# Kernel tuning notes

Hardware: AMD Instinct MI355X
Metric: run time of the kernel (lower is better)

## Reference

```python
import jax, jax.numpy as jnp
import numpy as np

EMBED_DIM = 768
N_HEADS = 12
HEAD_DIM = EMBED_DIM // N_HEADS
B, T = 2, 4096


def setup_inputs() -> dict:
    key = jax.random.key(0)
    k1, k2, k3, k4, k5 = jax.random.split(key, 5)
    s = 1.0 / np.sqrt(EMBED_DIM)
    return {
        "x": jax.random.normal(k1, (B, T, EMBED_DIM), dtype=jnp.float32),
        "Wqkv": jax.random.normal(k2, (EMBED_DIM, 3 * EMBED_DIM), dtype=jnp.float32) * s,
        "bqkv": jnp.zeros((3 * EMBED_DIM,), dtype=jnp.float32),
        "Wproj": jax.random.normal(k3, (EMBED_DIM, EMBED_DIM), dtype=jnp.float32) * s,
        "bproj": jnp.zeros((EMBED_DIM,), dtype=jnp.float32),
    }


def reference(x, Wqkv, bqkv, Wproj, bproj):
    Bz, Tz, C = x.shape
    qkv = x @ Wqkv + bqkv                         # [B,T,3C]
    q, k, v = jnp.split(qkv, 3, axis=2)
    # [B,T,H,D] -> [B,H,T,D]
    def heads(t):
        return t.reshape(Bz, Tz, N_HEADS, HEAD_DIM).transpose(0, 2, 1, 3)
    q, k, v = heads(q), heads(k), heads(v)
    scale = 1.0 / np.sqrt(HEAD_DIM)
    att = jnp.einsum("bhqd,bhkd->bhqk", q, k) * scale   # [B,H,T,T]
    causal = jnp.tril(jnp.ones((Tz, Tz), dtype=bool))
    att = jnp.where(causal[None, None], att, -jnp.inf)
    att = jax.nn.softmax(att, axis=-1)
    y = jnp.einsum("bhqk,bhkd->bhqd", att, v)            # [B,H,T,D]
    y = y.transpose(0, 2, 1, 3).reshape(Bz, Tz, C)
    return y @ Wproj + bproj
```

## Files before the change

kernel.cpp:

```cpp
#include <hip/hip_runtime.h>
#include <math.h>
#include <stdint.h>

typedef __attribute__((ext_vector_type(8))) short bf16x8;
typedef __attribute__((ext_vector_type(4))) float f32x4;

__device__ __forceinline__ unsigned short f2bf(float f) {
    union { float f; unsigned u; } v; v.f = f;
    return (unsigned short)((v.u + 0x7fffu + ((v.u >> 16) & 1u)) >> 16);
}

__device__ __forceinline__ unsigned pkbf(float a, float b) {
    union { float f; unsigned u; } x, y; x.f = a; y.f = b;
    return ((y.u + 0x8000u) & 0xffff0000u) | ((x.u + 0x8000u) >> 16);
}

__global__ void k_convert(const float* __restrict__ in, unsigned short* __restrict__ out, int n4) {
    int i = blockIdx.x * blockDim.x + threadIdx.x;
    if (i >= n4) return;
    float4 f = ((const float4*)in)[i];
    ushort4 o;
    o.x = f2bf(f.x); o.y = f2bf(f.y); o.z = f2bf(f.z); o.w = f2bf(f.w);
    ((ushort4*)out)[i] = o;
}

__global__ void k_transpose(const float* __restrict__ in, unsigned short* __restrict__ out, int R, int C) {
    __shared__ float tile[32][33];
    int c0 = blockIdx.x * 32, r0 = blockIdx.y * 32;
    int tx = threadIdx.x, ty = threadIdx.y;
#pragma unroll
    for (int i = 0; i < 4; ++i)
        tile[ty + i * 8][tx] = in[(size_t)(r0 + ty + i * 8) * C + c0 + tx];
    __syncthreads();
#pragma unroll
    for (int i = 0; i < 4; ++i)
        out[(size_t)(c0 + ty + i * 8) * R + r0 + tx] = f2bf(tile[tx][ty + i * 8]);
}

#define LDT 40

__device__ __forceinline__ void gemm_core(
    const unsigned short* __restrict__ A, const unsigned short* __restrict__ Bt,
    int K, unsigned short* As, unsigned short* Bs, f32x4 (&acc)[4][4])
{
    const int tid  = threadIdx.x;
    const int lane = tid & 63;
    const int w    = tid >> 6;
    const int wm   = (w >> 1) * 64, wn = (w & 1) * 64;
    const int l15  = lane & 15, quad = lane >> 4;
    const int m0 = blockIdx.x * 128, n0 = blockIdx.y * 128;

    const f32x4 zero = {0.f, 0.f, 0.f, 0.f};
#pragma unroll
    for (int i = 0; i < 4; ++i)
#pragma unroll
        for (int j = 0; j < 4; ++j) acc[i][j] = zero;

    const int r0 = tid >> 2, p8 = (tid & 3) * 8;
    const unsigned short* Ag0 = A  + (size_t)(m0 + r0) * K + p8;
    const unsigned short* Ag1 = A  + (size_t)(m0 + r0 + 64) * K + p8;
    const unsigned short* Bg0 = Bt + (size_t)(n0 + r0) * K + p8;
    const unsigned short* Bg1 = Bt + (size_t)(n0 + r0 + 64) * K + p8;

    int4 a0 = *(const int4*)Ag0;
    int4 a1 = *(const int4*)Ag1;
    int4 b0 = *(const int4*)Bg0;
    int4 b1 = *(const int4*)Bg1;

    const int nk = K >> 5;
    for (int kt = 0; kt < nk; ++kt) {
        __syncthreads();
        *(int4*)&As[r0 * LDT + p8]        = a0;
        *(int4*)&As[(r0 + 64) * LDT + p8] = a1;
        *(int4*)&Bs[r0 * LDT + p8]        = b0;
        *(int4*)&Bs[(r0 + 64) * LDT + p8] = b1;
        __syncthreads();
        if (kt + 1 < nk) {
            int koff = (kt + 1) * 32;
            a0 = *(const int4*)(Ag0 + koff);
            a1 = *(const int4*)(Ag1 + koff);
            b0 = *(const int4*)(Bg0 + koff);
            b1 = *(const int4*)(Bg1 + koff);
        }
        bf16x8 af[4], bfr[4];
#pragma unroll
        for (int mi = 0; mi < 4; ++mi)
            af[mi] = *(const bf16x8*)&As[(wm + mi * 16 + l15) * LDT + quad * 8];
#pragma unroll
        for (int nj = 0; nj < 4; ++nj)
            bfr[nj] = *(const bf16x8*)&Bs[(wn + nj * 16 + l15) * LDT + quad * 8];
#pragma unroll
        for (int mi = 0; mi < 4; ++mi)
#pragma unroll
            for (int nj = 0; nj < 4; ++nj)
                acc[mi][nj] = __builtin_amdgcn_mfma_f32_16x16x32_bf16(af[mi], bfr[nj], acc[mi][nj], 0, 0, 0);
    }
}

__global__ __launch_bounds__(256) void k_gemm_qkv(
    const unsigned short* __restrict__ A, const unsigned short* __restrict__ Bt,
    const float* __restrict__ bias,
    unsigned short* __restrict__ QL, unsigned short* __restrict__ KL,
    unsigned short* __restrict__ VL)
{
    __shared__ __align__(16) unsigned short As[128 * LDT];
    __shared__ __align__(16) unsigned short Bs[128 * LDT];
    f32x4 acc[4][4];
    gemm_core(A, Bt, 768, As, Bs, acc);

    const int tid = threadIdx.x, lane = tid & 63, w = tid >> 6;
    const int wm = (w >> 1) * 64, wn = (w & 1) * 64;
    const int l15 = lane & 15, quad = lane >> 4;
    const int m0 = blockIdx.x * 128, n0 = blockIdx.y * 128;
    const float cscale = 0.18033688011f;
#pragma unroll
    for (int nj = 0; nj < 4; ++nj) {
        int cg = n0 + wn + nj * 16 + l15;
        float bv = bias[cg];
        int which = cg / 768;
        int rem = cg - which * 768;
        int hd = rem >> 6, d = rem & 63;
        float sc = (which == 0) ? cscale : 1.0f;
#pragma unroll
        for (int mi = 0; mi < 4; ++mi) {
#pragma unroll
            for (int r = 0; r < 4; ++r) {
                int rg = m0 + wm + mi * 16 + quad * 4 + r;
                int b = rg >> 12, tk = rg & 4095;
                int bh = b * 12 + hd;
                unsigned short ob = f2bf((acc[mi][nj][r] + bv) * sc);
                if (which == 0) {
                    size_t idx = ((((size_t)bh * 128 + (tk >> 5)) * 2 + ((tk >> 4) & 1)) * 2 + (d >> 5)) * 512
                               + ((d >> 3) & 3) * 128 + (tk & 15) * 8 + (d & 7);
                    QL[idx] = ob;
                } else if (which == 1) {
                    size_t idx = ((((size_t)bh * 64 + (tk >> 6)) * 4 + ((tk >> 4) & 3)) * 2 + (d >> 5)) * 512
                               + ((d >> 3) & 3) * 128 + (tk & 15) * 8 + (d & 7);
                    KL[idx] = ob;
                } else {
                    int wi = tk & 63;
                    size_t idx = ((((size_t)bh * 64 + (tk >> 6)) * 4 + (d >> 4)) * 2 + (wi >> 5)) * 512
                               + ((wi >> 3) & 3) * 128 + (d & 15) * 8 + (wi & 7);
                    VL[idx] = ob;
                }
            }
        }
    }
}

__global__ __launch_bounds__(256) void k_gemm_proj(
    const unsigned short* __restrict__ A, const unsigned short* __restrict__ Bt,
    const float* __restrict__ bias, float* __restrict__ out)
{
    __shared__ __align__(16) unsigned short As[128 * LDT];
    __shared__ __align__(16) unsigned short Bs[128 * LDT];
    f32x4 acc[4][4];
    gemm_core(A, Bt, 768, As, Bs, acc);

    const int tid = threadIdx.x, lane = tid & 63, w = tid >> 6;
    const int wm = (w >> 1) * 64, wn = (w & 1) * 64;
    const int l15 = lane & 15, quad = lane >> 4;
    const int m0 = blockIdx.x * 128, n0 = blockIdx.y * 128;
#pragma unroll
    for (int nj = 0; nj < 4; ++nj) {
        int cg = n0 + wn + nj * 16 + l15;
        float bv = bias[cg];
#pragma unroll
        for (int mi = 0; mi < 4; ++mi)
#pragma unroll
            for (int r = 0; r < 4; ++r) {
                int rg = m0 + wm + mi * 16 + quad * 4 + r;
                out[(size_t)rg * 768 + cg] = acc[mi][nj][r] + bv;
            }
    }
}

#define LDP 68

__global__ __launch_bounds__(256) void k_attn(
    const unsigned short* __restrict__ QL, const unsigned short* __restrict__ KL,
    const unsigned short* __restrict__ VL, unsigned short* __restrict__ Y)
{
    __shared__ __align__(16) char smem[30720];
    unsigned short* Ps = (unsigned short*)smem;
    float* Cb = (float*)smem;

    const int tid = threadIdx.x, lane = tid & 63, w = tid >> 6;
    const int l15 = lane & 15, quad = lane >> 4;
    const int id = blockIdx.x;
    const int bh = id % 24;
    const int qi = 127 - id / 24;
    const int q0 = qi * 32;
    const int nkt = qi / 2 + 1;
    const int lo = (nkt * w) >> 2, hi = (nkt * (w + 1)) >> 2;
    unsigned short* Pw = Ps + w * 32 * LDP;

    const unsigned short* Qb = QL + (((size_t)bh * 128 + qi) * 4) * 512 + lane * 8;
    const unsigned short* Kb = KL + ((size_t)bh * 64) * 8 * 512 + lane * 8;
    const unsigned short* Vb = VL + ((size_t)bh * 64) * 8 * 512 + lane * 8;

    bf16x8 qt[2][2];
#pragma unroll
    for (int m = 0; m < 2; ++m)
#pragma unroll
        for (int h = 0; h < 2; ++h)
            qt[m][h] = *(const bf16x8*)(Qb + (m * 2 + h) * 512);

    const f32x4 zero = {0.f, 0.f, 0.f, 0.f};
    f32x4 O[2][4], lac[2];
#pragma unroll
    for (int m = 0; m < 2; ++m) {
        lac[m] = zero;
#pragma unroll
        for (int dj = 0; dj < 4; ++dj) O[m][dj] = zero;
    }

    const short ONE = (short)0x3F80;
    const bf16x8 onesf = {ONE, ONE, ONE, ONE, ONE, ONE, ONE, ONE};

    if (lo < hi) {
        bf16x8 ka[4][2];
#pragma unroll
        for (int i = 0; i < 4; ++i)
#pragma unroll
            for (int h = 0; h < 2; ++h)
                ka[i][h] = *(const bf16x8*)(Kb + ((size_t)lo * 8 + i * 2 + h) * 512);

        for (int kt = lo; kt < hi; ++kt) {
            const int kbase = kt * 64;

            f32x4 st[2][4];
#pragma unroll
            for (int i = 0; i < 4; ++i)
#pragma unroll
                for (int m = 0; m < 2; ++m) {
                    f32x4 z = __builtin_amdgcn_mfma_f32_16x16x32_bf16(ka[i][0], qt[m][0], zero, 0, 0, 0);
                    st[m][i] = __builtin_amdgcn_mfma_f32_16x16x32_bf16(ka[i][1], qt[m][1], z, 0, 0, 0);
                }

            bf16x8 vf[4][2];
#pragma unroll
            for (int dj = 0; dj < 4; ++dj)
#pragma unroll
                for (int h = 0; h < 2; ++h)
                    vf[dj][h] = *(const bf16x8*)(Vb + ((size_t)kt * 8 + dj * 2 + h) * 512);

            if (kt + 1 < hi) {
#pragma unroll
                for (int i = 0; i < 4; ++i)
#pragma unroll
                    for (int h = 0; h < 2; ++h)
                        ka[i][h] = *(const bf16x8*)(Kb + ((size_t)(kt + 1) * 8 + i * 2 + h) * 512);
            }

            if (kt == nkt - 1) {
#pragma unroll
                for (int m = 0; m < 2; ++m)
#pragma unroll
                    for (int i = 0; i < 4; ++i)
#pragma unroll
                        for (int r = 0; r < 4; ++r)
                            if (kbase + i * 16 + quad * 4 + r > q0 + m * 16 + l15)
                                st[m][i][r] = -INFINITY;
            }

#pragma unroll
            for (int m = 0; m < 2; ++m)
#pragma unroll
                for (int i = 0; i < 4; ++i) {
                    float p0 = exp2f(fminf(st[m][i][0], 80.f));
                    float p1 = exp2f(fminf(st[m][i][1], 80.f));
                    float p2 = exp2f(fminf(st[m][i][2], 80.f));
                    float p3 = exp2f(fminf(st[m][i][3], 80.f));
                    uint2 pk; pk.x = pkbf(p0, p1); pk.y = pkbf(p2, p3);
                    *(uint2*)&Pw[(size_t)(m * 16 + l15) * LDP + i * 16 + quad * 4] = pk;
                }

            bf16x8 pa[2][2];
#pragma unroll
            for (int m = 0; m < 2; ++m) {
                pa[m][0] = *(const bf16x8*)&Pw[(size_t)(m * 16 + l15) * LDP + quad * 8];
                pa[m][1] = *(const bf16x8*)&Pw[(size_t)(m * 16 + l15) * LDP + 32 + quad * 8];
            }

#pragma unroll
            for (int m = 0; m < 2; ++m) {
                f32x4 z = __builtin_amdgcn_mfma_f32_16x16x32_bf16(pa[m][0], onesf, lac[m], 0, 0, 0);
                lac[m] = __builtin_amdgcn_mfma_f32_16x16x32_bf16(pa[m][1], onesf, z, 0, 0, 0);
            }
#pragma unroll
            for (int dj = 0; dj < 4; ++dj)
#pragma unroll
                for (int m = 0; m < 2; ++m) {
                    f32x4 z = __builtin_amdgcn_mfma_f32_16x16x32_bf16(pa[m][0], vf[dj][0], O[m][dj], 0, 0, 0);
                    O[m][dj] = __builtin_amdgcn_mfma_f32_16x16x32_bf16(pa[m][1], vf[dj][1], z, 0, 0, 0);
                }
        }
    }

    __syncthreads();
    if (w > 0) {
        float* Ow = Cb + (w - 1) * 2560;
#pragma unroll
        for (int m = 0; m < 2; ++m) {
#pragma unroll
            for (int dj = 0; dj < 4; ++dj)
                *(f32x4*)&Ow[(m * 4 + dj) * 256 + lane * 4] = O[m][dj];
            *(f32x4*)&Ow[2048 + m * 256 + lane * 4] = lac[m];
        }
    }
    __syncthreads();
    if (w == 0) {
#pragma unroll
        for (int c = 0; c < 3; ++c) {
            const float* Ow = Cb + c * 2560;
#pragma unroll
            for (int m = 0; m < 2; ++m) {
#pragma unroll
                for (int dj = 0; dj < 4; ++dj)
                    O[m][dj] += *(const f32x4*)&Ow[(m * 4 + dj) * 256 + lane * 4];
                lac[m] += *(const f32x4*)&Ow[2048 + m * 256 + lane * 4];
            }
        }
        const int b = bh / 12, hd = bh % 12;
#pragma unroll
        for (int m = 0; m < 2; ++m)
#pragma unroll
            for (int r = 0; r < 4; ++r) {
                float inv = 1.0f / lac[m][r];
                int t = q0 + 16 * m + quad * 4 + r;
                size_t base = ((size_t)(b * 4096 + t)) * 768 + hd * 64;
#pragma unroll
                for (int dj = 0; dj < 4; ++dj)
                    Y[base + dj * 16 + l15] = f2bf(O[m][dj][r] * inv);
            }
    }
}

extern "C" void kernel_launch(void* const* d_in, const int* in_sizes, int n_in,
                              void* d_out, int out_size, void* d_ws, size_t ws_size,
                              hipStream_t stream) {
    (void)in_sizes; (void)n_in; (void)out_size; (void)ws_size;
    const float* x     = (const float*)d_in[0];
    const float* Wqkv  = (const float*)d_in[1];
    const float* bqkv  = (const float*)d_in[2];
    const float* Wproj = (const float*)d_in[3];
    const float* bproj = (const float*)d_in[4];
    float* out = (float*)d_out;

    char* ws = (char*)d_ws;
    size_t off = 0;
    auto alloc = [&](size_t bytes) -> void* {
        void* p = ws + off;
        off += (bytes + 255) & ~(size_t)255;
        return p;
    };
    unsigned short* xb     = (unsigned short*)alloc((size_t)8192 * 768 * 2);
    unsigned short* WqkvT  = (unsigned short*)alloc((size_t)2304 * 768 * 2);
    unsigned short* WprojT = (unsigned short*)alloc((size_t)768 * 768 * 2);
    unsigned short* QLb    = (unsigned short*)alloc((size_t)24 * 4096 * 64 * 2);
    unsigned short* KLb    = (unsigned short*)alloc((size_t)24 * 4096 * 64 * 2);
    unsigned short* VLb    = (unsigned short*)alloc((size_t)24 * 4096 * 64 * 2);
    unsigned short* Yb     = (unsigned short*)alloc((size_t)8192 * 768 * 2);

    k_convert<<<6144, 256, 0, stream>>>(x, xb, 8192 * 768 / 4);
    dim3 tb(32, 8);
    k_transpose<<<dim3(72, 24), tb, 0, stream>>>(Wqkv, WqkvT, 768, 2304);
    k_transpose<<<dim3(24, 24), tb, 0, stream>>>(Wproj, WprojT, 768, 768);
    k_gemm_qkv<<<dim3(64, 18), 256, 0, stream>>>(xb, WqkvT, bqkv, QLb, KLb, VLb);
    k_attn<<<dim3(3072), 256, 0, stream>>>(QLb, KLb, VLb, Yb);
    k_gemm_proj<<<dim3(64, 6), 256, 0, stream>>>(Yb, WprojT, bproj, out);
}
```

Baseline: 271.8 us.

## Use direct global-to-LDS loads in GEMM and streamline attention softmax packing

The GEMM core now uses global_load_lds to copy tiles straight into shared memory instead of staging them through registers. This drops the register prefetch, so loads are no longer overlapped with compute, and the LDS row stride goes from 40 to 32, which may raise bank conflicts. The attention kernel switches to the hardware exp2 builtin and packs bf16 with v_perm. It also moves K/V pointers incrementally, makes the wave index scalar via readfirstlane, and widens the P-tile stride to 72. These changes aim to cut VALU and address arithmetic.

```diff
diff --git a/kernel.cpp b/kernel.cpp
--- a/kernel.cpp
+++ b/kernel.cpp
@@ -10,9 +10,10 @@
     return (unsigned short)((v.u + 0x7fffu + ((v.u >> 16) & 1u)) >> 16);
 }
 
-__device__ __forceinline__ unsigned pkbf(float a, float b) {
-    union { float f; unsigned u; } x, y; x.f = a; y.f = b;
-    return ((y.u + 0x8000u) & 0xffff0000u) | ((x.u + 0x8000u) >> 16);
+__device__ __forceinline__ void gld_lds16(const void* g, void* l) {
+    __builtin_amdgcn_global_load_lds(
+        (const __attribute__((address_space(1))) unsigned*)(uintptr_t)g,
+        (__attribute__((address_space(3))) unsigned*)(uintptr_t)l, 16, 0, 0);
 }
 
 __global__ void k_convert(const float* __restrict__ in, unsigned short* __restrict__ out, int n4) {
@@ -37,7 +38,7 @@
         out[(size_t)(c0 + ty + i * 8) * R + r0 + tx] = f2bf(tile[tx][ty + i * 8]);
 }
 
-#define LDT 40
+#define LDT 32
 
 __device__ __forceinline__ void gemm_core(
     const unsigned short* __restrict__ A, const unsigned short* __restrict__ Bt,
@@ -61,27 +62,20 @@
     const unsigned short* Ag1 = A  + (size_t)(m0 + r0 + 64) * K + p8;
     const unsigned short* Bg0 = Bt + (size_t)(n0 + r0) * K + p8;
     const unsigned short* Bg1 = Bt + (size_t)(n0 + r0 + 64) * K + p8;
-
-    int4 a0 = *(const int4*)Ag0;
-    int4 a1 = *(const int4*)Ag1;
-    int4 b0 = *(const int4*)Bg0;
-    int4 b1 = *(const int4*)Bg1;
+    unsigned short* lA0 = As + r0 * LDT + p8;
+    unsigned short* lA1 = lA0 + 64 * LDT;
+    unsigned short* lB0 = Bs + r0 * LDT + p8;
+    unsigned short* lB1 = lB0 + 64 * LDT;
 
     const int nk = K >> 5;
     for (int kt = 0; kt < nk; ++kt) {
         __syncthreads();
-        *(int4*)&As[r0 * LDT + p8]        = a0;
-        *(int4*)&As[(r0 + 64) * LDT + p8] = a1;
-        *(int4*)&Bs[r0 * LDT + p8]        = b0;
-        *(int4*)&Bs[(r0 + 64) * LDT + p8] = b1;
+        gld_lds16(Ag0, lA0);
+        gld_lds16(Ag1, lA1);
+        gld_lds16(Bg0, lB0);
+        gld_lds16(Bg1, lB1);
+        Ag0 += 32; Ag1 += 32; Bg0 += 32; Bg1 += 32;
         __syncthreads();
-        if (kt + 1 < nk) {
-            int koff = (kt + 1) * 32;
-            a0 = *(const int4*)(Ag0 + koff);
-            a1 = *(const int4*)(Ag1 + koff);
-            b0 = *(const int4*)(Bg0 + koff);
-            b1 = *(const int4*)(Bg1 + koff);
-        }
         bf16x8 af[4], bfr[4];
 #pragma unroll
         for (int mi = 0; mi < 4; ++mi)
@@ -175,7 +169,7 @@
     }
 }
 
-#define LDP 68
+#define LDP 72
 
 __global__ __launch_bounds__(256) void k_attn(
     const unsigned short* __restrict__ QL, const unsigned short* __restrict__ KL,
@@ -185,7 +179,8 @@
     unsigned short* Ps = (unsigned short*)smem;
     float* Cb = (float*)smem;
 
-    const int tid = threadIdx.x, lane = tid & 63, w = tid >> 6;
+    const int tid = threadIdx.x, lane = tid & 63;
+    const int w = __builtin_amdgcn_readfirstlane(tid >> 6);
     const int l15 = lane & 15, quad = lane >> 4;
     const int id = blockIdx.x;
     const int bh = id % 24;
@@ -195,9 +190,12 @@
     const int lo = (nkt * w) >> 2, hi = (nkt * (w + 1)) >> 2;
     unsigned short* Pw = Ps + w * 32 * LDP;
 
+    unsigned short* pwb = Pw + l15 * LDP + quad * 4;
+    const unsigned short* prb = Pw + l15 * LDP + quad * 8;
+
     const unsigned short* Qb = QL + (((size_t)bh * 128 + qi) * 4) * 512 + lane * 8;
-    const unsigned short* Kb = KL + ((size_t)bh * 64) * 8 * 512 + lane * 8;
-    const unsigned short* Vb = VL + ((size_t)bh * 64) * 8 * 512 + lane * 8;
+    const unsigned short* kp = KL + ((size_t)bh * 64 + lo) * 8 * 512 + lane * 8;
+    const unsigned short* vp = VL + ((size_t)bh * 64 + lo) * 8 * 512 + lane * 8;
 
     bf16x8 qt[2][2];
 #pragma unroll
@@ -224,11 +222,9 @@
         for (int i = 0; i < 4; ++i)
 #pragma unroll
             for (int h = 0; h < 2; ++h)
-                ka[i][h] = *(const bf16x8*)(Kb + ((size_t)lo * 8 + i * 2 + h) * 512);
+                ka[i][h] = *(const bf16x8*)(kp + (i * 2 + h) * 512);
 
         for (int kt = lo; kt < hi; ++kt) {
-            const int kbase = kt * 64;
-
             f32x4 st[2][4];
 #pragma unroll
             for (int i = 0; i < 4; ++i)
@@ -243,24 +239,27 @@
             for (int dj = 0; dj < 4; ++dj)
 #pragma unroll
                 for (int h = 0; h < 2; ++h)
-                    vf[dj][h] = *(const bf16x8*)(Vb + ((size_t)kt * 8 + dj * 2 + h) * 512);
+                    vf[dj][h] = *(const bf16x8*)(vp + (dj * 2 + h) * 512);
+            vp += 8 * 512;
 
             if (kt + 1 < hi) {
+                kp += 8 * 512;
 #pragma unroll
                 for (int i = 0; i < 4; ++i)
 #pragma unroll
                     for (int h = 0; h < 2; ++h)
-                        ka[i][h] = *(const bf16x8*)(Kb + ((size_t)(kt + 1) * 8 + i * 2 + h) * 512);
+                        ka[i][h] = *(const bf16x8*)(kp + (i * 2 + h) * 512);
             }
 
             if (kt == nkt - 1) {
+                const int kb = kt * 64;
 #pragma unroll
                 for (int m = 0; m < 2; ++m)
 #pragma unroll
                     for (int i = 0; i < 4; ++i)
 #pragma unroll
                         for (int r = 0; r < 4; ++r)
-                            if (kbase + i * 16 + quad * 4 + r > q0 + m * 16 + l15)
+                            if (kb + i * 16 + quad * 4 + r > q0 + m * 16 + l15)
                                 st[m][i][r] = -INFINITY;
             }
 
@@ -268,19 +267,21 @@
             for (int m = 0; m < 2; ++m)
 #pragma unroll
                 for (int i = 0; i < 4; ++i) {
-                    float p0 = exp2f(fminf(st[m][i][0], 80.f));
-                    float p1 = exp2f(fminf(st[m][i][1], 80.f));
-                    float p2 = exp2f(fminf(st[m][i][2], 80.f));
-                    float p3 = exp2f(fminf(st[m][i][3], 80.f));
-                    uint2 pk; pk.x = pkbf(p0, p1); pk.y = pkbf(p2, p3);
-                    *(uint2*)&Pw[(size_t)(m * 16 + l15) * LDP + i * 16 + quad * 4] = pk;
+                    unsigned e0 = __float_as_uint(__builtin_amdgcn_exp2f(fminf(st[m][i][0], 80.f))) + 0x8000u;
+                    unsigned e1 = __float_as_uint(__builtin_amdgcn_exp2f(fminf(st[m][i][1], 80.f))) + 0x8000u;
+                    unsigned e2 = __float_as_uint(__builtin_amdgcn_exp2f(fminf(st[m][i][2], 80.f))) + 0x8000u;
+                    unsigned e3 = __float_as_uint(__builtin_amdgcn_exp2f(fminf(st[m][i][3], 80.f))) + 0x8000u;
+                    uint2 pk;
+                    pk.x = __builtin_amdgcn_perm(e1, e0, 0x07060302);
+                    pk.y = __builtin_amdgcn_perm(e3, e2, 0x07060302);
+                    *(uint2*)(pwb + m * 16 * LDP + i * 16) = pk;
                 }
 
             bf16x8 pa[2][2];
 #pragma unroll
             for (int m = 0; m < 2; ++m) {
-                pa[m][0] = *(const bf16x8*)&Pw[(size_t)(m * 16 + l15) * LDP + quad * 8];
-                pa[m][1] = *(const bf16x8*)&Pw[(size_t)(m * 16 + l15) * LDP + 32 + quad * 8];
+                pa[m][0] = *(const bf16x8*)(prb + m * 16 * LDP);
+                pa[m][1] = *(const bf16x8*)(prb + m * 16 * LDP + 32);
             }
 
 #pragma unroll
```

Measured after the change: 262.2 us. -3.5%, faster.
